# Performance work log

Hardware: AMD Instinct MI355X
Metric: run time of the kernel (lower is better)

Reference implementation:

```python
import jax, jax.numpy as jnp
import numpy as np

C_IN = 128
C_QK = C_IN // 8


def setup_inputs() -> dict:
    key = jax.random.key(0)
    kx, kq, kk, kv = jax.random.split(key, 4)
    x = jax.random.normal(kx, (8, C_IN, 64, 64), dtype=jnp.float32)
    # 1x1 conv weights, stored as (c_out, c_in); fan-in scaled init
    s = 1.0 / np.sqrt(C_IN)
    Wq = jax.random.normal(kq, (C_QK, C_IN), dtype=jnp.float32) * s
    Wk = jax.random.normal(kk, (C_QK, C_IN), dtype=jnp.float32) * s
    Wv = jax.random.normal(kv, (C_IN, C_IN), dtype=jnp.float32) * s
    gamma = jnp.ones((1,), dtype=jnp.float32) * 0.5  # nonzero so residual branch matters
    return {"x": x, "Wq": Wq, "Wk": Wk, "Wv": Wv, "gamma": gamma}


def reference(x, Wq, Wk, Wv, gamma):
    b, c, h, w = x.shape
    xt = rearr = x.reshape(b, c, h * w)            # b c n
    q = jnp.einsum('oc,bcn->bno', Wq, xt)          # b n c//8
    k = jnp.einsum('oc,bcn->bon', Wk, xt)          # b c//8 n
    v = jnp.einsum('oc,bcn->bno', Wv, xt)          # b n c
    energy = jnp.einsum('bno,bom->bnm', q, k)      # b n n (no scale, per source)
    attn = jax.nn.softmax(energy, axis=-1)
    out = jnp.einsum('bnm,bmc->bnc', attn, v)      # b n c
    out = out.transpose(0, 2, 1).reshape(b, c, h, w)
    return x + gamma[0] * out
```

## Files before the change

### kernel.cpp

```cpp
#include <hip/hip_runtime.h>
#include <hip/hip_bf16.h>


typedef __bf16 bf16x8 __attribute__((ext_vector_type(8)));
typedef __bf16 bf16x4 __attribute__((ext_vector_type(4)));
typedef float  f32x16 __attribute__((ext_vector_type(16)));

static constexpr int Bb = 8, Cc = 128, Nn = 4096, CQ = 16;

__device__ __forceinline__ f32x16 mfma32(bf16x8 a, bf16x8 b, f32x16 c) {
    return __builtin_amdgcn_mfma_f32_32x32x16_bf16(a, b, c, 0, 0, 0);
}
struct HL { __bf16 h, l; };
__device__ __forceinline__ HL hilo(float f) {
    HL r;
    r.h = (__bf16)f;
    r.l = (__bf16)(f - (float)r.h);
    return r;
}

__global__ __launch_bounds__(320) void qkv_kernel(
    const float* __restrict__ x, const float* __restrict__ Wq,
    const float* __restrict__ Wk, const float* __restrict__ Wv,
    __bf16* __restrict__ qw, __bf16* __restrict__ kw, __bf16* __restrict__ vw)
{
    const int b = blockIdx.y, tile = blockIdx.x, n0 = tile * 32, t = threadIdx.x;
    const int wave = t >> 6, lane = t & 63, lr = lane & 31, lq = lane >> 5;

    __shared__ __bf16 xh[32][136], xl[32][136];
    __shared__ __bf16 sc[4][32][40];

    if (t < 256) {
        const int n = t & 31, ci0 = (t >> 5) * 16;
        float v[16];
        #pragma unroll
        for (int k = 0; k < 16; ++k)
            v[k] = x[((size_t)(b * Cc + ci0 + k)) * Nn + n0 + n];
        bf16x8 h8[2], l8[2];
        #pragma unroll
        for (int k = 0; k < 16; ++k) {
            HL z = hilo(v[k]);
            h8[k >> 3][k & 7] = z.h;
            l8[k >> 3][k & 7] = z.l;
        }
        *(bf16x8*)&xh[n][ci0]     = h8[0];
        *(bf16x8*)&xh[n][ci0 + 8] = h8[1];
        *(bf16x8*)&xl[n][ci0]     = l8[0];
        *(bf16x8*)&xl[n][ci0 + 8] = l8[1];
    }
    __syncthreads();

    if (wave == 4) {
        const float* wrow = (lr < 16) ? (Wq + (size_t)lr * Cc)
                                      : (Wk + (size_t)(lr - 16) * Cc);
        f32x16 acc = {};
        #pragma unroll
        for (int ks = 0; ks < 8; ++ks) {
            float4 w0 = *(const float4*)(wrow + ks * 16 + lq * 8);
            float4 w1 = *(const float4*)(wrow + ks * 16 + lq * 8 + 4);
            bf16x8 ah, al;
            HL z;
            z = hilo(w0.x); ah[0] = z.h; al[0] = z.l;
            z = hilo(w0.y); ah[1] = z.h; al[1] = z.l;
            z = hilo(w0.z); ah[2] = z.h; al[2] = z.l;
            z = hilo(w0.w); ah[3] = z.h; al[3] = z.l;
            z = hilo(w1.x); ah[4] = z.h; al[4] = z.l;
            z = hilo(w1.y); ah[5] = z.h; al[5] = z.l;
            z = hilo(w1.z); ah[6] = z.h; al[6] = z.l;
            z = hilo(w1.w); ah[7] = z.h; al[7] = z.l;
            bf16x8 bh = *(const bf16x8*)&xh[lr][ks * 16 + lq * 8];
            bf16x8 bl = *(const bf16x8*)&xl[lr][ks * 16 + lq * 8];
            acc = mfma32(ah, bh, acc);
            acc = mfma32(al, bh, acc);
            acc = mfma32(ah, bl, acc);
        }
        __bf16* qb = qw + (((size_t)b * 128 + tile) << 10);
        __bf16* kb = kw + (((size_t)b * 128 + tile) << 10);
        #pragma unroll
        for (int rg = 0; rg < 4; ++rg) {
            bf16x4 h4, l4;
            #pragma unroll
            for (int j = 0; j < 4; ++j) {
                float v = acc[rg * 4 + j];
                if (rg < 2) v *= 1.44269504089f;
                HL z = hilo(v);
                h4[j] = z.h; l4[j] = z.l;
            }
            const int off = (rg & 1) * 256 + lr * 8 + 4 * lq;
            __bf16* base = (rg < 2) ? qb : kb;
            *(bf16x4*)(base + off) = h4;
            *(bf16x4*)(base + 512 + off) = l4;
        }
    } else {
        const int ct = wave;
        f32x16 acc = {};
        #pragma unroll
        for (int ks = 0; ks < 8; ++ks) {
            const float* wp = Wv + (size_t)(ct * 32 + lr) * Cc + ks * 16 + lq * 8;
            float4 w0 = *(const float4*)wp;
            float4 w1 = *(const float4*)(wp + 4);
            bf16x8 a = { (__bf16)w0.x, (__bf16)w0.y, (__bf16)w0.z, (__bf16)w0.w,
                         (__bf16)w1.x, (__bf16)w1.y, (__bf16)w1.z, (__bf16)w1.w };
            bf16x8 bh = *(const bf16x8*)&xh[lr][ks * 16 + lq * 8];
            acc = mfma32(a, bh, acc);
        }
        const int klr = (lr & ~12) | ((lr & 4) << 1) | ((lr & 8) >> 1);
        #pragma unroll
        for (int r = 0; r < 16; ++r) {
            int crow = (r & 3) + 8 * (r >> 2) + 4 * lq;
            sc[wave][crow][klr] = (__bf16)acc[r];
        }
        __bf16* vb = vw + (((size_t)b * 128 + tile) << 12) + ct * 1024;
        #pragma unroll
        for (int u = 0; u < 2; ++u) {
            bf16x8 row = *(const bf16x8*)&sc[wave][lr][u * 16 + lq * 8];
            *(bf16x8*)(vb + u * 512 + lane * 8) = row;
        }
    }
}

__global__ __launch_bounds__(512, 4) void attn_kernel(
    const float* __restrict__ x, const __bf16* __restrict__ qw,
    const __bf16* __restrict__ kw, const __bf16* __restrict__ vw,
    const float* __restrict__ gamma, float* __restrict__ out)
{
    const int h = blockIdx.x;
    const int b = h & 7;
    const int qt = h >> 3;
    const int t = threadIdx.x;
    const int wave = t >> 6, lane = t & 63, lr = lane & 31, lq = lane >> 5;
    const int kr = wave & 3, ch = wave >> 2;

    __shared__ float accbuf[32][129];
    __shared__ float lbuf[32];

    const __bf16* qb = qw + (((size_t)b * 128 + qt) << 10) + lane * 8;
    const bf16x8 qhi = *(const bf16x8*)qb;
    const bf16x8 qlo = *(const bf16x8*)(qb + 512);

    const int c0 = kr * 32;
    const __bf16* kp = kw + (((size_t)b * 128 + c0) << 10) + lane * 8;
    const __bf16* vp = vw + (((size_t)b * 128 + c0) << 12) + ch * 2048 + lane * 8;

    f32x16 acc0 = {}, acc1 = {};
    float l_part = 0.f;

    bf16x8 akh = *(const bf16x8*)kp,          akl = *(const bf16x8*)(kp + 512);
    bf16x8 av0 = *(const bf16x8*)vp,          av1 = *(const bf16x8*)(vp + 512);
    bf16x8 av2 = *(const bf16x8*)(vp + 1024), av3 = *(const bf16x8*)(vp + 1536);
    bf16x8 bkh, bkl, bv0, bv1, bv2, bv3;

    auto body = [&](const bf16x8& Kh, const bf16x8& Kl, const bf16x8& V0,
                    const bf16x8& V1, const bf16x8& V2, const bf16x8& V3) {
        f32x16 s = {};
        s = mfma32(Kh, qhi, s);
        s = mfma32(Kl, qhi, s);
        s = mfma32(Kh, qlo, s);

        float p[16];
        #pragma unroll
        for (int r = 0; r < 16; ++r) p[r] = __builtin_amdgcn_exp2f(s[r]);
        l_part += ((((p[0] + p[1]) + (p[2] + p[3])) + ((p[4] + p[5]) + (p[6] + p[7])))
                 + (((p[8] + p[9]) + (p[10] + p[11])) + ((p[12] + p[13]) + (p[14] + p[15]))));

        bf16x8 F0, F1;
        #pragma unroll
        for (int j = 0; j < 8; ++j) {
            F0[j] = (__bf16)p[j];
            F1[j] = (__bf16)p[8 + j];
        }

        acc0 = mfma32(V0, F0, acc0);
        acc0 = mfma32(V1, F1, acc0);
        acc1 = mfma32(V2, F0, acc1);
        acc1 = mfma32(V3, F1, acc1);
    };

    for (int it = 0; it < 15; ++it) {
        kp += 1024; vp += 4096;
        bkh = *(const bf16x8*)kp;          bkl = *(const bf16x8*)(kp + 512);
        bv0 = *(const bf16x8*)vp;          bv1 = *(const bf16x8*)(vp + 512);
        bv2 = *(const bf16x8*)(vp + 1024); bv3 = *(const bf16x8*)(vp + 1536);
        body(akh, akl, av0, av1, av2, av3);
        kp += 1024; vp += 4096;
        akh = *(const bf16x8*)kp;          akl = *(const bf16x8*)(kp + 512);
        av0 = *(const bf16x8*)vp;          av1 = *(const bf16x8*)(vp + 512);
        av2 = *(const bf16x8*)(vp + 1024); av3 = *(const bf16x8*)(vp + 1536);
        body(bkh, bkl, bv0, bv1, bv2, bv3);
    }
    kp += 1024; vp += 4096;
    bkh = *(const bf16x8*)kp;          bkl = *(const bf16x8*)(kp + 512);
    bv0 = *(const bf16x8*)vp;          bv1 = *(const bf16x8*)(vp + 512);
    bv2 = *(const bf16x8*)(vp + 1024); bv3 = *(const bf16x8*)(vp + 1536);
    body(akh, akl, av0, av1, av2, av3);
    body(bkh, bkl, bv0, bv1, bv2, bv3);

    l_part += __shfl_xor(l_part, 32);

    if (kr == 0) {
        #pragma unroll
        for (int r = 0; r < 16; ++r) {
            int c = ch * 64 + (r & 3) + 8 * (r >> 2) + 4 * lq;
            accbuf[lr][c] = acc0[r];
            accbuf[lr][c + 32] = acc1[r];
        }
        if (wave == 0 && lane < 32) lbuf[lr] = l_part;
    }
    __syncthreads();
    if (kr != 0) {
        #pragma unroll
        for (int r = 0; r < 16; ++r) {
            int c = ch * 64 + (r & 3) + 8 * (r >> 2) + 4 * lq;
            atomicAdd(&accbuf[lr][c], acc0[r]);
            atomicAdd(&accbuf[lr][c + 32], acc1[r]);
        }
        if (ch == 0 && lane < 32) atomicAdd(&lbuf[lr], l_part);
    }
    __syncthreads();

    const float g = gamma[0];
    const int q = t & 31, cg = t >> 5;
    const float linv = 1.0f / lbuf[q];
    const int n0b = qt * 32;
    #pragma unroll
    for (int i = 0; i < 8; ++i) {
        int c = cg + 16 * i;
        size_t idx = ((size_t)(b * Cc + c)) * Nn + n0b + q;
        out[idx] = x[idx] + g * accbuf[q][c] * linv;
    }
}

extern "C" void kernel_launch(void* const* d_in, const int* in_sizes, int n_in,
                              void* d_out, int out_size, void* d_ws, size_t ws_size,
                              hipStream_t stream) {
    const float* x  = (const float*)d_in[0];
    const float* Wq = (const float*)d_in[1];
    const float* Wk = (const float*)d_in[2];
    const float* Wv = (const float*)d_in[3];
    const float* gm = (const float*)d_in[4];

    __bf16* qw = (__bf16*)d_ws;
    __bf16* kw = qw + (size_t)Bb * 128 * 1024;
    __bf16* vw = kw + (size_t)Bb * 128 * 1024;

    qkv_kernel<<<dim3(Nn / 32, Bb), 320, 0, stream>>>(x, Wq, Wk, Wv, qw, kw, vw);
    attn_kernel<<<dim3(Nn / 32 * Bb), 512, 0, stream>>>(x, qw, kw, vw, gm,
                                                        (float*)d_out);
}
```

Measured before the change: 187.9 us.

## Give each attention block 64 queries with full-channel accumulators per wave

The attention kernel now gives each block two 32-query tiles instead of one. Each wave computes the scores for its key slice once and accumulates all 128 output channels, where before two waves split the channels and each recomputed the same QK scores and exp. This halves the redundant score/exp work and halves the grid. In exchange each wave holds four accumulators and loads eight V fragments per step without double-buffering, which raises register pressure. It also doubles the shared-memory reduction buffer, which may hurt occupancy under launch bounds of 4 blocks.

```diff
diff --git a/kernel.cpp b/kernel.cpp
--- a/kernel.cpp
+++ b/kernel.cpp
@@ -126,32 +126,34 @@
 {
     const int h = blockIdx.x;
     const int b = h & 7;
-    const int qt = h >> 3;
+    const int qp = h >> 3;
     const int t = threadIdx.x;
     const int wave = t >> 6, lane = t & 63, lr = lane & 31, lq = lane >> 5;
-    const int kr = wave & 3, ch = wave >> 2;
-
-    __shared__ float accbuf[32][129];
-    __shared__ float lbuf[32];
-
-    const __bf16* qb = qw + (((size_t)b * 128 + qt) << 10) + lane * 8;
+    const int kr = wave & 3, qh = wave >> 2;
+
+    __shared__ float accbuf[64][129];
+    __shared__ float lbuf[64];
+
+    const int tile = qp * 2 + qh;
+    const __bf16* qb = qw + (((size_t)b * 128 + tile) << 10) + lane * 8;
     const bf16x8 qhi = *(const bf16x8*)qb;
     const bf16x8 qlo = *(const bf16x8*)(qb + 512);
 
     const int c0 = kr * 32;
     const __bf16* kp = kw + (((size_t)b * 128 + c0) << 10) + lane * 8;
-    const __bf16* vp = vw + (((size_t)b * 128 + c0) << 12) + ch * 2048 + lane * 8;
-
-    f32x16 acc0 = {}, acc1 = {};
+    const __bf16* vp = vw + (((size_t)b * 128 + c0) << 12) + lane * 8;
+
+    f32x16 acc[4] = {{}, {}, {}, {}};
     float l_part = 0.f;
 
-    bf16x8 akh = *(const bf16x8*)kp,          akl = *(const bf16x8*)(kp + 512);
-    bf16x8 av0 = *(const bf16x8*)vp,          av1 = *(const bf16x8*)(vp + 512);
-    bf16x8 av2 = *(const bf16x8*)(vp + 1024), av3 = *(const bf16x8*)(vp + 1536);
-    bf16x8 bkh, bkl, bv0, bv1, bv2, bv3;
-
-    auto body = [&](const bf16x8& Kh, const bf16x8& Kl, const bf16x8& V0,
-                    const bf16x8& V1, const bf16x8& V2, const bf16x8& V3) {
+    bf16x8 akh = *(const bf16x8*)kp, akl = *(const bf16x8*)(kp + 512);
+    bf16x8 bkh, bkl;
+
+    auto body = [&](const bf16x8& Kh, const bf16x8& Kl, const __bf16* vpc) {
+        bf16x8 v[8];
+        #pragma unroll
+        for (int u = 0; u < 8; ++u) v[u] = *(const bf16x8*)(vpc + u * 512);
+
         f32x16 s = {};
         s = mfma32(Kh, qhi, s);
         s = mfma32(Kl, qhi, s);
@@ -170,61 +172,59 @@
             F1[j] = (__bf16)p[8 + j];
         }
 
-        acc0 = mfma32(V0, F0, acc0);
-        acc0 = mfma32(V1, F1, acc0);
-        acc1 = mfma32(V2, F0, acc1);
-        acc1 = mfma32(V3, F1, acc1);
+        #pragma unroll
+        for (int ct = 0; ct < 4; ++ct) {
+            acc[ct] = mfma32(v[2 * ct],     F0, acc[ct]);
+            acc[ct] = mfma32(v[2 * ct + 1], F1, acc[ct]);
+        }
     };
 
     for (int it = 0; it < 15; ++it) {
-        kp += 1024; vp += 4096;
-        bkh = *(const bf16x8*)kp;          bkl = *(const bf16x8*)(kp + 512);
-        bv0 = *(const bf16x8*)vp;          bv1 = *(const bf16x8*)(vp + 512);
-        bv2 = *(const bf16x8*)(vp + 1024); bv3 = *(const bf16x8*)(vp + 1536);
-        body(akh, akl, av0, av1, av2, av3);
-        kp += 1024; vp += 4096;
-        akh = *(const bf16x8*)kp;          akl = *(const bf16x8*)(kp + 512);
-        av0 = *(const bf16x8*)vp;          av1 = *(const bf16x8*)(vp + 512);
-        av2 = *(const bf16x8*)(vp + 1024); av3 = *(const bf16x8*)(vp + 1536);
-        body(bkh, bkl, bv0, bv1, bv2, bv3);
-    }
-    kp += 1024; vp += 4096;
-    bkh = *(const bf16x8*)kp;          bkl = *(const bf16x8*)(kp + 512);
-    bv0 = *(const bf16x8*)vp;          bv1 = *(const bf16x8*)(vp + 512);
-    bv2 = *(const bf16x8*)(vp + 1024); bv3 = *(const bf16x8*)(vp + 1536);
-    body(akh, akl, av0, av1, av2, av3);
-    body(bkh, bkl, bv0, bv1, bv2, bv3);
+        kp += 1024;
+        bkh = *(const bf16x8*)kp; bkl = *(const bf16x8*)(kp + 512);
+        body(akh, akl, vp); vp += 4096;
+        kp += 1024;
+        akh = *(const bf16x8*)kp; akl = *(const bf16x8*)(kp + 512);
+        body(bkh, bkl, vp); vp += 4096;
+    }
+    kp += 1024;
+    bkh = *(const bf16x8*)kp; bkl = *(const bf16x8*)(kp + 512);
+    body(akh, akl, vp); vp += 4096;
+    body(bkh, bkl, vp);
 
     l_part += __shfl_xor(l_part, 32);
 
+    const int qrow = qh * 32 + lr;
     if (kr == 0) {
         #pragma unroll
-        for (int r = 0; r < 16; ++r) {
-            int c = ch * 64 + (r & 3) + 8 * (r >> 2) + 4 * lq;
-            accbuf[lr][c] = acc0[r];
-            accbuf[lr][c + 32] = acc1[r];
-        }
-        if (wave == 0 && lane < 32) lbuf[lr] = l_part;
+        for (int ct = 0; ct < 4; ++ct)
+            #pragma unroll
+            for (int r = 0; r < 16; ++r) {
+                int c = (r & 3) + 8 * (r >> 2) + 4 * lq + 32 * ct;
+                accbuf[qrow][c] = acc[ct][r];
+            }
+        if (lane < 32) lbuf[qrow] = l_part;
     }
     __syncthreads();
     if (kr != 0) {
         #pragma unroll
-        for (int r = 0; r < 16; ++r) {
-            int c = ch * 64 + (r & 3) + 8 * (r >> 2) + 4 * lq;
-            atomicAdd(&accbuf[lr][c], acc0[r]);
-            atomicAdd(&accbuf[lr][c + 32], acc1[r]);
-        }
-        if (ch == 0 && lane < 32) atomicAdd(&lbuf[lr], l_part);
+        for (int ct = 0; ct < 4; ++ct)
+            #pragma unroll
+            for (int r = 0; r < 16; ++r) {
+                int c = (r & 3) + 8 * (r >> 2) + 4 * lq + 32 * ct;
+                atomicAdd(&accbuf[qrow][c], acc[ct][r]);
+            }
+        if (lane < 32) atomicAdd(&lbuf[qrow], l_part);
     }
     __syncthreads();
 
     const float g = gamma[0];
-    const int q = t & 31, cg = t >> 5;
+    const int q = t & 63, cg = t >> 6;
     const float linv = 1.0f / lbuf[q];
-    const int n0b = qt * 32;
+    const int n0b = qp * 64;
     #pragma unroll
-    for (int i = 0; i < 8; ++i) {
-        int c = cg + 16 * i;
+    for (int i = 0; i < 16; ++i) {
+        int c = cg + 8 * i;
         size_t idx = ((size_t)(b * Cc + c)) * Nn + n0b + q;
         out[idx] = x[idx] + g * accbuf[q][c] * linv;
     }
@@ -244,6 +244,6 @@
     __bf16* vw = kw + (size_t)Bb * 128 * 1024;
 
     qkv_kernel<<<dim3(Nn / 32, Bb), 320, 0, stream>>>(x, Wq, Wk, Wv, qw, kw, vw);
-    attn_kernel<<<dim3(Nn / 32 * Bb), 512, 0, stream>>>(x, qw, kw, vw, gm,
+    attn_kernel<<<dim3(Nn / 64 * Bb), 512, 0, stream>>>(x, qw, kw, vw, gm,
                                                         (float*)d_out);
 }
```

Measured after the change: 224.5 us. 1.2x slower.

## Widen QKV tiles to 64 columns and triple-buffer K/V loads in attention

Applied to the files above, without the earlier changes.

The projection kernel now processes 64 spatial positions per block with 384 threads. Two waves compute Q/K for each 32-column half, and four waves loop over both halves for V, so the weight loads and conversions are amortized over twice as many columns and only half as many blocks are launched. The attention loop moves from double to triple buffering of K/V register sets, issuing loads two chunks ahead to hide global latency. The cost is higher register pressure in the attention kernel, which runs at 4 blocks of 512 threads, and more LDS per projection block.

```diff
diff --git a/kernel.cpp b/kernel.cpp
--- a/kernel.cpp
+++ b/kernel.cpp
@@ -19,38 +19,36 @@
     return r;
 }
 
-__global__ __launch_bounds__(320) void qkv_kernel(
+__global__ __launch_bounds__(384) void qkv_kernel(
     const float* __restrict__ x, const float* __restrict__ Wq,
     const float* __restrict__ Wk, const float* __restrict__ Wv,
     __bf16* __restrict__ qw, __bf16* __restrict__ kw, __bf16* __restrict__ vw)
 {
-    const int b = blockIdx.y, tile = blockIdx.x, n0 = tile * 32, t = threadIdx.x;
+    const int b = blockIdx.y, tb = blockIdx.x, n0 = tb * 64, t = threadIdx.x;
     const int wave = t >> 6, lane = t & 63, lr = lane & 31, lq = lane >> 5;
 
-    __shared__ __bf16 xh[32][136], xl[32][136];
+    __shared__ __bf16 xh[64][136], xl[64][136];
     __shared__ __bf16 sc[4][32][40];
 
     if (t < 256) {
-        const int n = t & 31, ci0 = (t >> 5) * 16;
-        float v[16];
-        #pragma unroll
-        for (int k = 0; k < 16; ++k)
-            v[k] = x[((size_t)(b * Cc + ci0 + k)) * Nn + n0 + n];
-        bf16x8 h8[2], l8[2];
-        #pragma unroll
-        for (int k = 0; k < 16; ++k) {
-            HL z = hilo(v[k]);
-            h8[k >> 3][k & 7] = z.h;
-            l8[k >> 3][k & 7] = z.l;
-        }
-        *(bf16x8*)&xh[n][ci0]     = h8[0];
-        *(bf16x8*)&xh[n][ci0 + 8] = h8[1];
-        *(bf16x8*)&xl[n][ci0]     = l8[0];
-        *(bf16x8*)&xl[n][ci0 + 8] = l8[1];
+        const int n = lane, ci0 = (t >> 6) * 32;
+        #pragma unroll
+        for (int g = 0; g < 4; ++g) {
+            float v[8];
+            #pragma unroll
+            for (int k = 0; k < 8; ++k)
+                v[k] = x[((size_t)(b * Cc + ci0 + g * 8 + k)) * Nn + n0 + n];
+            bf16x8 h8, l8;
+            #pragma unroll
+            for (int k = 0; k < 8; ++k) { HL z = hilo(v[k]); h8[k] = z.h; l8[k] = z.l; }
+            *(bf16x8*)&xh[n][ci0 + g * 8] = h8;
+            *(bf16x8*)&xl[n][ci0 + g * 8] = l8;
+        }
     }
     __syncthreads();
 
-    if (wave == 4) {
+    if (wave < 2) {
+        const int nh = wave;
         const float* wrow = (lr < 16) ? (Wq + (size_t)lr * Cc)
                                       : (Wk + (size_t)(lr - 16) * Cc);
         f32x16 acc = {};
@@ -68,12 +66,13 @@
             z = hilo(w1.y); ah[5] = z.h; al[5] = z.l;
             z = hilo(w1.z); ah[6] = z.h; al[6] = z.l;
             z = hilo(w1.w); ah[7] = z.h; al[7] = z.l;
-            bf16x8 bh = *(const bf16x8*)&xh[lr][ks * 16 + lq * 8];
-            bf16x8 bl = *(const bf16x8*)&xl[lr][ks * 16 + lq * 8];
+            bf16x8 bh = *(const bf16x8*)&xh[nh * 32 + lr][ks * 16 + lq * 8];
+            bf16x8 bl = *(const bf16x8*)&xl[nh * 32 + lr][ks * 16 + lq * 8];
             acc = mfma32(ah, bh, acc);
             acc = mfma32(al, bh, acc);
             acc = mfma32(ah, bl, acc);
         }
+        const int tile = tb * 2 + nh;
         __bf16* qb = qw + (((size_t)b * 128 + tile) << 10);
         __bf16* kb = kw + (((size_t)b * 128 + tile) << 10);
         #pragma unroll
@@ -92,29 +91,32 @@
             *(bf16x4*)(base + 512 + off) = l4;
         }
     } else {
-        const int ct = wave;
-        f32x16 acc = {};
-        #pragma unroll
-        for (int ks = 0; ks < 8; ++ks) {
-            const float* wp = Wv + (size_t)(ct * 32 + lr) * Cc + ks * 16 + lq * 8;
-            float4 w0 = *(const float4*)wp;
-            float4 w1 = *(const float4*)(wp + 4);
-            bf16x8 a = { (__bf16)w0.x, (__bf16)w0.y, (__bf16)w0.z, (__bf16)w0.w,
-                         (__bf16)w1.x, (__bf16)w1.y, (__bf16)w1.z, (__bf16)w1.w };
-            bf16x8 bh = *(const bf16x8*)&xh[lr][ks * 16 + lq * 8];
-            acc = mfma32(a, bh, acc);
-        }
+        const int ct = wave - 2;
         const int klr = (lr & ~12) | ((lr & 4) << 1) | ((lr & 8) >> 1);
-        #pragma unroll
-        for (int r = 0; r < 16; ++r) {
-            int crow = (r & 3) + 8 * (r >> 2) + 4 * lq;
-            sc[wave][crow][klr] = (__bf16)acc[r];
-        }
-        __bf16* vb = vw + (((size_t)b * 128 + tile) << 12) + ct * 1024;
-        #pragma unroll
-        for (int u = 0; u < 2; ++u) {
-            bf16x8 row = *(const bf16x8*)&sc[wave][lr][u * 16 + lq * 8];
-            *(bf16x8*)(vb + u * 512 + lane * 8) = row;
+        for (int nh = 0; nh < 2; ++nh) {
+            f32x16 acc = {};
+            #pragma unroll
+            for (int ks = 0; ks < 8; ++ks) {
+                const float* wp = Wv + (size_t)(ct * 32 + lr) * Cc + ks * 16 + lq * 8;
+                float4 w0 = *(const float4*)wp;
+                float4 w1 = *(const float4*)(wp + 4);
+                bf16x8 a = { (__bf16)w0.x, (__bf16)w0.y, (__bf16)w0.z, (__bf16)w0.w,
+                             (__bf16)w1.x, (__bf16)w1.y, (__bf16)w1.z, (__bf16)w1.w };
+                bf16x8 bh = *(const bf16x8*)&xh[nh * 32 + lr][ks * 16 + lq * 8];
+                acc = mfma32(a, bh, acc);
+            }
+            #pragma unroll
+            for (int r = 0; r < 16; ++r) {
+                int crow = (r & 3) + 8 * (r >> 2) + 4 * lq;
+                sc[ct][crow][klr] = (__bf16)acc[r];
+            }
+            const int chunk = tb * 2 + nh;
+            __bf16* vb = vw + (((size_t)b * 128 + chunk) << 12) + ct * 1024;
+            #pragma unroll
+            for (int u = 0; u < 2; ++u) {
+                bf16x8 row = *(const bf16x8*)&sc[ct][lr][u * 16 + lq * 8];
+                *(bf16x8*)(vb + u * 512 + lane * 8) = row;
+            }
         }
     }
 }
@@ -145,10 +147,16 @@
     f32x16 acc0 = {}, acc1 = {};
     float l_part = 0.f;
 
-    bf16x8 akh = *(const bf16x8*)kp,          akl = *(const bf16x8*)(kp + 512);
-    bf16x8 av0 = *(const bf16x8*)vp,          av1 = *(const bf16x8*)(vp + 512);
-    bf16x8 av2 = *(const bf16x8*)(vp + 1024), av3 = *(const bf16x8*)(vp + 1536);
+    bf16x8 akh, akl, av0, av1, av2, av3;
     bf16x8 bkh, bkl, bv0, bv1, bv2, bv3;
+    bf16x8 ckh, ckl, cv0, cv1, cv2, cv3;
+
+#define LOADSET(KH, KL, V0, V1, V2, V3, c) {                          \
+        const __bf16* kpc = kp + (size_t)(c) * 1024;                  \
+        const __bf16* vpc = vp + (size_t)(c) * 4096;                  \
+        KH = *(const bf16x8*)kpc;          KL = *(const bf16x8*)(kpc + 512);  \
+        V0 = *(const bf16x8*)vpc;          V1 = *(const bf16x8*)(vpc + 512);  \
+        V2 = *(const bf16x8*)(vpc + 1024); V3 = *(const bf16x8*)(vpc + 1536); }
 
     auto body = [&](const bf16x8& Kh, const bf16x8& Kl, const bf16x8& V0,
                     const bf16x8& V1, const bf16x8& V2, const bf16x8& V3) {
@@ -176,24 +184,19 @@
         acc1 = mfma32(V3, F1, acc1);
     };
 
-    for (int it = 0; it < 15; ++it) {
-        kp += 1024; vp += 4096;
-        bkh = *(const bf16x8*)kp;          bkl = *(const bf16x8*)(kp + 512);
-        bv0 = *(const bf16x8*)vp;          bv1 = *(const bf16x8*)(vp + 512);
-        bv2 = *(const bf16x8*)(vp + 1024); bv3 = *(const bf16x8*)(vp + 1536);
+    LOADSET(akh, akl, av0, av1, av2, av3, 0);
+    LOADSET(bkh, bkl, bv0, bv1, bv2, bv3, 1);
+    for (int it = 0; it < 10; ++it) {
+        LOADSET(ckh, ckl, cv0, cv1, cv2, cv3, 3 * it + 2);
         body(akh, akl, av0, av1, av2, av3);
-        kp += 1024; vp += 4096;
-        akh = *(const bf16x8*)kp;          akl = *(const bf16x8*)(kp + 512);
-        av0 = *(const bf16x8*)vp;          av1 = *(const bf16x8*)(vp + 512);
-        av2 = *(const bf16x8*)(vp + 1024); av3 = *(const bf16x8*)(vp + 1536);
+        LOADSET(akh, akl, av0, av1, av2, av3, 3 * it + 3);
         body(bkh, bkl, bv0, bv1, bv2, bv3);
-    }
-    kp += 1024; vp += 4096;
-    bkh = *(const bf16x8*)kp;          bkl = *(const bf16x8*)(kp + 512);
-    bv0 = *(const bf16x8*)vp;          bv1 = *(const bf16x8*)(vp + 512);
-    bv2 = *(const bf16x8*)(vp + 1024); bv3 = *(const bf16x8*)(vp + 1536);
+        LOADSET(bkh, bkl, bv0, bv1, bv2, bv3, 3 * it + 4);
+        body(ckh, ckl, cv0, cv1, cv2, cv3);
+    }
     body(akh, akl, av0, av1, av2, av3);
     body(bkh, bkl, bv0, bv1, bv2, bv3);
+#undef LOADSET
 
     l_part += __shfl_xor(l_part, 32);
 
@@ -243,7 +246,7 @@
     __bf16* kw = qw + (size_t)Bb * 128 * 1024;
     __bf16* vw = kw + (size_t)Bb * 128 * 1024;
 
-    qkv_kernel<<<dim3(Nn / 32, Bb), 320, 0, stream>>>(x, Wq, Wk, Wv, qw, kw, vw);
+    qkv_kernel<<<dim3(Nn / 64, Bb), 384, 0, stream>>>(x, Wq, Wk, Wv, qw, kw, vw);
     attn_kernel<<<dim3(Nn / 32 * Bb), 512, 0, stream>>>(x, qw, kw, vw, gm,
                                                         (float*)d_out);
 }
```

Result: slower. 614.3 us (+227.0%).
